# Kernel tuning notes

Hardware: AMD Instinct MI355X
Metric: run time of the kernel (lower is better)

The kernel has to match this reference:

```python
import jax, jax.numpy as jnp
import numpy as np

HIDDEN = 256
IN = 72  # 9*8
NUM_STEPS = 8


def setup_inputs() -> dict:
    key = jax.random.key(0)
    ks = jax.random.split(key, 12)
    s = 1.0 / np.sqrt(HIDDEN)
    B = 32768
    return {
        "z": jax.random.normal(ks[0], (1, B, HIDDEN), dtype=jnp.float32),
        # LSTM (torch layout): gates order i, f, g, o
        "W_ih": jax.random.uniform(ks[1], (4 * HIDDEN, IN), minval=-s, maxval=s),
        "W_hh": jax.random.uniform(ks[2], (4 * HIDDEN, HIDDEN), minval=-s, maxval=s),
        "b_ih": jax.random.uniform(ks[3], (4 * HIDDEN,), minval=-s, maxval=s),
        "b_hh": jax.random.uniform(ks[4], (4 * HIDDEN,), minval=-s, maxval=s),
        # Linear h: 256 -> 256
        "Wh": jax.random.uniform(ks[5], (HIDDEN, HIDDEN), minval=-s, maxval=s),
        "bh": jax.random.uniform(ks[6], (HIDDEN,), minval=-s, maxval=s),
        # Linear c: 256 -> 256
        "Wc": jax.random.uniform(ks[7], (HIDDEN, HIDDEN), minval=-s, maxval=s),
        "bc": jax.random.uniform(ks[8], (HIDDEN,), minval=-s, maxval=s),
        # Linear hout: 256 -> 72
        "Wo": jax.random.uniform(ks[9], (IN, HIDDEN), minval=-s, maxval=s),
        "bo": jax.random.uniform(ks[10], (IN,), minval=-s, maxval=s),
    }


def reference(z, W_ih, W_hh, b_ih, b_hh, Wh, bh, Wc, bc, Wo, bo):
    B = z.shape[1]
    z0 = z[0]                           # (B, 256)
    h = z0 @ Wh.T + bh                  # initial hidden state
    c = z0 @ Wc.T + bc                  # initial cell state
    x = jnp.zeros((B, IN), dtype=z.dtype)

    def step(carry, _):
        x, h, c = carry
        gates = x @ W_ih.T + b_ih + h @ W_hh.T + b_hh   # (B, 1024)
        i, f, g, o = jnp.split(gates, 4, axis=-1)
        i = jax.nn.sigmoid(i)
        f = jax.nn.sigmoid(f)
        g = jnp.tanh(g)
        o = jax.nn.sigmoid(o)
        c = f * c + i * g
        h = o * jnp.tanh(c)
        y = jax.nn.sigmoid(h @ Wo.T + bo)               # (B, 72), fed back as next input
        return (y, h, c), y

    _, ys = jax.lax.scan(step, (x, h, c), None, length=NUM_STEPS)  # (8, B, 72)
    return jnp.transpose(ys, (1, 0, 2))                             # (B, 8, 72)
```

## Files before the change

### kernel.cpp

```cpp
#include <hip/hip_runtime.h>
#include <hip/hip_bf16.h>

#define HID   256
#define NGATE 1024
#define INP   72
#define STEPS 8
#define TB    64
#define NTHR  1024
#define LDH   264
#define LDX   104

#define WSEQ2 32768
#define OFF_WHI 524288
#define OFF_WCI 589824
#define N_ALL   655360
#define OFF_BG_BYTES    1310720
#define OFF_STAGE_BYTES 1314816

typedef short  s8_t  __attribute__((ext_vector_type(8)));
typedef float  f4_t  __attribute__((ext_vector_type(4)));

static __device__ __forceinline__ unsigned short f2bf(float f) {
  unsigned int u = __float_as_uint(f);
  u = (u + 0x7FFFu + ((u >> 16) & 1u)) >> 16;
  return (unsigned short)u;
}
static __device__ __forceinline__ float fast_rcp(float x) {
#if __has_builtin(__builtin_amdgcn_rcpf)
  return __builtin_amdgcn_rcpf(x);
#else
  return 1.f / x;
#endif
}
static __device__ __forceinline__ float sigm(float x) {
  return fast_rcp(1.f + __expf(-x));
}
static __device__ __forceinline__ float tanh_(float x) {
  float t = fminf(-2.f * x, 88.f);
  float e = __expf(t);
  return (1.f - e) * fast_rcp(1.f + e);
}

__global__ void prep_kernel(const float* __restrict__ Wih, const float* __restrict__ Whh,
                            const float* __restrict__ bih, const float* __restrict__ bhh,
                            const float* __restrict__ Wh, const float* __restrict__ Wc,
                            const float* __restrict__ Wo,
                            unsigned short* __restrict__ wsh, float* __restrict__ bg) {
  int stride = gridDim.x * blockDim.x;
  for (int i = blockIdx.x * blockDim.x + threadIdx.x; i < N_ALL + NGATE; i += stride) {
    if (i < N_ALL) {
      float v = 0.f;
      if (i < OFF_WHI) {
        int w  = i >> 15;
        int r  = i & 32767;
        int f  = r >> 9;
        int e  = r & 511;
        int lane = e >> 3, j = e & 7;
        int lq = lane >> 4, ln = lane & 15;
        int kk = lq * 8 + j;
        if (f < 32) {
          int kc = f >> 2, q = f & 3;
          int g  = q * 256 + w * 16 + ln;
          int k  = kc * 32 + kk;
          v = Whh[g * HID + k];
        } else if (f < 44) {
          int t  = f - 32;
          int kc = t >> 2, q = t & 3;
          int g  = q * 256 + w * 16 + ln;
          int k  = kc * 32 + kk;
          v = (k < INP) ? Wih[g * INP + k] : 0.f;
        } else if (f < 52) {
          int kc = f - 44;
          int c  = w * 16 + ln;
          int k  = kc * 32 + kk;
          v = (w < 5 && c < INP) ? Wo[c * HID + k] : 0.f;
        }
      } else {
        int base = (i < OFF_WCI) ? OFF_WHI : OFF_WCI;
        const float* Wsrc = (i < OFF_WCI) ? Wh : Wc;
        int jj = i - base;
        int w  = jj >> 12;
        int r  = jj & 4095;
        int kc = r >> 9;
        int e  = r & 511;
        int lane = e >> 3, j = e & 7;
        int lq = lane >> 4, ln = lane & 15;
        int c  = w * 16 + ln;
        int k  = kc * 32 + lq * 8 + j;
        v = Wsrc[c * HID + k];
      }
      wsh[i] = f2bf(v);
    } else {
      int jb = i - N_ALL;
      bg[jb] = bih[jb] + bhh[jb];
    }
  }
}

template <int STAGED>
__global__ __launch_bounds__(NTHR, 4) void lstm_kernel(
    const float* __restrict__ z, const unsigned short* __restrict__ wsh,
    const float* __restrict__ bg, const float* __restrict__ bh,
    const float* __restrict__ bc, const float* __restrict__ bo,
    float* __restrict__ out, float* __restrict__ stage, int NB) {
  __shared__ unsigned short h_lds[TB * LDH];
  __shared__ unsigned short x_lds[TB * LDX];

  const int tid  = threadIdx.x;
  const int w    = tid >> 6;
  const int lane = tid & 63;
  const int lq   = lane >> 4;
  const int ln   = lane & 15;
  const int rb   = blockIdx.x * TB;
  const int colh0 = w * 16 + ln;

  const unsigned short* wst = wsh + w * WSEQ2 + lane * 8;
  const unsigned short* whi = wsh + OFF_WHI + w * 4096 + lane * 8;
  const unsigned short* wci = wsh + OFF_WCI + w * 4096 + lane * 8;
  const unsigned short* h_rd = &h_lds[ln * LDH + lq * 8];
  const unsigned short* x_rd = &x_lds[ln * LDX + lq * 8];
  unsigned short*       h_wr = &h_lds[(lq * 4) * LDH + colh0];

  for (int i = tid; i < TB * LDX; i += NTHR) x_lds[i] = 0;

  f4_t acc_h[4], acc_c[4];
  #pragma unroll
  for (int rt = 0; rt < 4; ++rt) {
    acc_h[rt] = {0.f, 0.f, 0.f, 0.f};
    acc_c[rt] = {0.f, 0.f, 0.f, 0.f};
  }

  const float* z_l = z + (size_t)(rb + ln) * HID + lq * 8;

  #pragma unroll 2
  for (int kc = 0; kc < 8; ++kc) {
    s8_t a[4];
    #pragma unroll
    for (int rt = 0; rt < 4; ++rt) {
      f4_t v0 = *reinterpret_cast<const f4_t*>(z_l + rt * 16 * HID + kc * 32);
      f4_t v1 = *reinterpret_cast<const f4_t*>(z_l + rt * 16 * HID + kc * 32 + 4);
      s8_t av;
      av[0] = (short)f2bf(v0[0]); av[1] = (short)f2bf(v0[1]);
      av[2] = (short)f2bf(v0[2]); av[3] = (short)f2bf(v0[3]);
      av[4] = (short)f2bf(v1[0]); av[5] = (short)f2bf(v1[1]);
      av[6] = (short)f2bf(v1[2]); av[7] = (short)f2bf(v1[3]);
      a[rt] = av;
    }
    s8_t bhf = *reinterpret_cast<const s8_t*>(whi + kc * 512);
    s8_t bcf = *reinterpret_cast<const s8_t*>(wci + kc * 512);
    #pragma unroll
    for (int rt = 0; rt < 4; ++rt) {
      acc_h[rt] = __builtin_amdgcn_mfma_f32_16x16x32_bf16(a[rt], bhf, acc_h[rt], 0, 0, 0);
      acc_c[rt] = __builtin_amdgcn_mfma_f32_16x16x32_bf16(a[rt], bcf, acc_c[rt], 0, 0, 0);
    }
  }

  float c_reg[4][4];
  {
    const float bhv = bh[colh0];
    const float bcv = bc[colh0];
    #pragma unroll
    for (int rt = 0; rt < 4; ++rt)
      #pragma unroll
      for (int r = 0; r < 4; ++r) {
        float hv = acc_h[rt][r] + bhv;
        c_reg[rt][r] = acc_c[rt][r] + bcv;
        h_wr[(rt * 16 + r) * LDH] = f2bf(hv);
      }
  }
  __syncthreads();

  float biasg[4];
  #pragma unroll
  for (int q = 0; q < 4; ++q)
    biasg[q] = bg[q * 256 + colh0];

  float bov = 0.f;
  if (w < 5 && colh0 < INP) bov = bo[colh0];

  for (int s = 0; s < STEPS; ++s) {
    f4_t acc[4][4];
    #pragma unroll
    for (int q = 0; q < 4; ++q)
      #pragma unroll
      for (int rt = 0; rt < 4; ++rt) {
        const float b = biasg[q];
        acc[q][rt] = {b, b, b, b};
      }

    #pragma unroll 2
    for (int kc = 0; kc < 8; ++kc) {
      s8_t a[4];
      #pragma unroll
      for (int rt = 0; rt < 4; ++rt)
        a[rt] = *reinterpret_cast<const s8_t*>(h_rd + rt * 16 * LDH + kc * 32);
      #pragma unroll
      for (int q = 0; q < 4; ++q) {
        s8_t bfr = *reinterpret_cast<const s8_t*>(wst + (kc * 4 + q) * 512);
        #pragma unroll
        for (int rt = 0; rt < 4; ++rt)
          acc[q][rt] = __builtin_amdgcn_mfma_f32_16x16x32_bf16(a[rt], bfr, acc[q][rt], 0, 0, 0);
      }
    }
    #pragma unroll
    for (int kc = 0; kc < 3; ++kc) {
      s8_t a[4];
      #pragma unroll
      for (int rt = 0; rt < 4; ++rt)
        a[rt] = *reinterpret_cast<const s8_t*>(x_rd + rt * 16 * LDX + kc * 32);
      #pragma unroll
      for (int q = 0; q < 4; ++q) {
        s8_t bfr = *reinterpret_cast<const s8_t*>(wst + (32 + kc * 4 + q) * 512);
        #pragma unroll
        for (int rt = 0; rt < 4; ++rt)
          acc[q][rt] = __builtin_amdgcn_mfma_f32_16x16x32_bf16(a[rt], bfr, acc[q][rt], 0, 0, 0);
      }
    }
    __syncthreads();

    #pragma unroll
    for (int rt = 0; rt < 4; ++rt)
      #pragma unroll
      for (int r = 0; r < 4; ++r) {
        float iv = sigm(acc[0][rt][r]);
        float fv = sigm(acc[1][rt][r]);
        float gv = tanh_(acc[2][rt][r]);
        float ov = sigm(acc[3][rt][r]);
        float cn = fv * c_reg[rt][r] + iv * gv;
        c_reg[rt][r] = cn;
        float hv = ov * tanh_(cn);
        h_wr[(rt * 16 + r) * LDH] = f2bf(hv);
      }
    __syncthreads();

    if (w < 5) {
      f4_t accy[4];
      #pragma unroll
      for (int rt = 0; rt < 4; ++rt) accy[rt] = {bov, bov, bov, bov};
      #pragma unroll 2
      for (int kc = 0; kc < 8; ++kc) {
        s8_t bfr = *reinterpret_cast<const s8_t*>(wst + (44 + kc) * 512);
        #pragma unroll
        for (int rt = 0; rt < 4; ++rt) {
          s8_t a = *reinterpret_cast<const s8_t*>(h_rd + rt * 16 * LDH + kc * 32);
          accy[rt] = __builtin_amdgcn_mfma_f32_16x16x32_bf16(a, bfr, accy[rt], 0, 0, 0);
        }
      }
      if (colh0 < INP) {
        float* st_base;
        if (STAGED) {
          st_base = stage + (((size_t)s * NB + blockIdx.x) * TB + lq * 4) * INP + colh0;
        } else {
          st_base = out + (size_t)(rb + lq * 4) * (STEPS * INP) + s * INP + colh0;
        }
        unsigned short* x_wr = &x_lds[(lq * 4) * LDX + colh0];
        #pragma unroll
        for (int rt = 0; rt < 4; ++rt)
          #pragma unroll
          for (int r = 0; r < 4; ++r) {
            float yv = sigm(accy[rt][r]);
            if (STAGED) {
              st_base[(size_t)(rt * 16 + r) * INP] = yv;
            } else {
              st_base[(size_t)(rt * 16 + r) * (STEPS * INP)] = yv;
            }
            x_wr[(rt * 16 + r) * LDX] = f2bf(yv);
          }
      }
    }
    __syncthreads();
  }
}

__global__ __launch_bounds__(512) void reorder_kernel(
    const float* __restrict__ stage, float* __restrict__ out, int NB) {
  const int lane = threadIdx.x & 63;
  const int row  = blockIdx.x * 8 + (threadIdx.x >> 6);
  const int b    = row >> 6;
  const int r    = row & 63;
  #pragma unroll
  for (int i = lane; i < STEPS * INP; i += 64) {
    int s = i / INP;
    int c = i - s * INP;
    out[(size_t)row * (STEPS * INP) + i] =
        stage[(((size_t)s * NB + b) * TB + r) * INP + c];
  }
}

extern "C" void kernel_launch(void* const* d_in, const int* in_sizes, int n_in,
                              void* d_out, int out_size, void* d_ws, size_t ws_size,
                              hipStream_t stream) {
  const float* z   = (const float*)d_in[0];
  const float* Wih = (const float*)d_in[1];
  const float* Whh = (const float*)d_in[2];
  const float* bih = (const float*)d_in[3];
  const float* bhh = (const float*)d_in[4];
  const float* Wh  = (const float*)d_in[5];
  const float* bh  = (const float*)d_in[6];
  const float* Wc  = (const float*)d_in[7];
  const float* bc  = (const float*)d_in[8];
  const float* Wo  = (const float*)d_in[9];
  const float* bo  = (const float*)d_in[10];
  float* out = (float*)d_out;

  unsigned short* wsh = (unsigned short*)d_ws;
  float* bg    = (float*)((char*)d_ws + OFF_BG_BYTES);
  float* stage = (float*)((char*)d_ws + OFF_STAGE_BYTES);

  const int B  = in_sizes[0] / HID;
  const int NB = B / TB;

  hipLaunchKernelGGL(prep_kernel, dim3(512), dim3(256), 0, stream,
                     Wih, Whh, bih, bhh, Wh, Wc, Wo, wsh, bg);

  const size_t stage_need = (size_t)OFF_STAGE_BYTES + (size_t)B * STEPS * INP * 4;
  if (ws_size >= stage_need) {
    hipLaunchKernelGGL((lstm_kernel<1>), dim3(NB), dim3(NTHR), 0, stream,
                       z, wsh, bg, bh, bc, bo, out, stage, NB);
    hipLaunchKernelGGL(reorder_kernel, dim3(B / 8), dim3(512), 0, stream,
                       stage, out, NB);
  } else {
    hipLaunchKernelGGL((lstm_kernel<0>), dim3(NB), dim3(NTHR), 0, stream,
                       z, wsh, bg, bh, bc, bo, out, stage, NB);
  }
}
```

Baseline: 557.0 us.

## Double-buffer LSTM hidden state in LDS to drop one barrier per step

Hidden state now ping-pongs between two LDS buffers, and the x buffer shares a unified LDS array with stride LDH. The h@W_hh product reads the current buffer and the new h is written to the other, so the barrier at the end of each step goes away and the x-part MFMAs now sit after the first barrier. The step loop is unrolled by two via a macro so buffer pointers are static. This raises LDS use (three 64x264 bf16 buffers), which could limit occupancy, and the synchronization correctness across steps is subtle.

```diff
diff --git a/kernel.cpp b/kernel.cpp
--- a/kernel.cpp
+++ b/kernel.cpp
@@ -8,7 +8,7 @@
 #define TB    64
 #define NTHR  1024
 #define LDH   264
-#define LDX   104
+#define ELEMS_BUF 16896
 
 #define WSEQ2 32768
 #define OFF_WHI 524288
@@ -97,14 +97,107 @@
   }
 }
 
+#define STEP(CUR_RD, NXT_RD, NXT_WR, SIDX)                                    \
+  {                                                                           \
+    f4_t acc[4][4];                                                           \
+    _Pragma("unroll")                                                         \
+    for (int q = 0; q < 4; ++q)                                               \
+      _Pragma("unroll")                                                       \
+      for (int rt = 0; rt < 4; ++rt) {                                        \
+        const float b = biasg[q];                                             \
+        acc[q][rt] = {b, b, b, b};                                            \
+      }                                                                       \
+     \
+    _Pragma("unroll 2")                                                       \
+    for (int kc = 0; kc < 8; ++kc) {                                          \
+      s8_t a[4];                                                              \
+      _Pragma("unroll")                                                       \
+      for (int rt = 0; rt < 4; ++rt)                                          \
+        a[rt] = *reinterpret_cast<const s8_t*>((CUR_RD) + rt * 16 * LDH + kc * 32); \
+      _Pragma("unroll")                                                       \
+      for (int q = 0; q < 4; ++q) {                                           \
+        s8_t bfr = *reinterpret_cast<const s8_t*>(wst + (kc * 4 + q) * 512);  \
+        _Pragma("unroll")                                                     \
+        for (int rt = 0; rt < 4; ++rt)                                        \
+          acc[q][rt] = __builtin_amdgcn_mfma_f32_16x16x32_bf16(a[rt], bfr, acc[q][rt], 0, 0, 0); \
+      }                                                                       \
+    }                                                                         \
+    __syncthreads();         \
+           \
+    _Pragma("unroll")                                                         \
+    for (int kc = 0; kc < 3; ++kc) {                                          \
+      s8_t a[4];                                                              \
+      _Pragma("unroll")                                                       \
+      for (int rt = 0; rt < 4; ++rt)                                          \
+        a[rt] = *reinterpret_cast<const s8_t*>(h_rdA + ELEMS_BUF + rt * 16 * LDH + kc * 32); \
+      _Pragma("unroll")                                                       \
+      for (int q = 0; q < 4; ++q) {                                           \
+        s8_t bfr = *reinterpret_cast<const s8_t*>(wst + (32 + kc * 4 + q) * 512); \
+        _Pragma("unroll")                                                     \
+        for (int rt = 0; rt < 4; ++rt)                                        \
+          acc[q][rt] = __builtin_amdgcn_mfma_f32_16x16x32_bf16(a[rt], bfr, acc[q][rt], 0, 0, 0); \
+      }                                                                       \
+    }                                                                         \
+       \
+    _Pragma("unroll")                                                         \
+    for (int rt = 0; rt < 4; ++rt)                                            \
+      _Pragma("unroll")                                                       \
+      for (int r = 0; r < 4; ++r) {                                           \
+        float iv = sigm(acc[0][rt][r]);                                       \
+        float fv = sigm(acc[1][rt][r]);                                       \
+        float gv = tanh_(acc[2][rt][r]);                                      \
+        float ov = sigm(acc[3][rt][r]);                                       \
+        float cn = fv * c_reg[rt][r] + iv * gv;                               \
+        c_reg[rt][r] = cn;                                                    \
+        float hv = ov * tanh_(cn);                                            \
+        (NXT_WR)[(rt * 16 + r) * LDH] = f2bf(hv);                             \
+      }                                                                       \
+    __syncthreads();                    \
+                       \
+    if (w < 5) {                                                              \
+      f4_t accy[4];                                                           \
+      _Pragma("unroll")                                                       \
+      for (int rt = 0; rt < 4; ++rt) accy[rt] = {bov, bov, bov, bov};         \
+      _Pragma("unroll 2")                                                     \
+      for (int kc = 0; kc < 8; ++kc) {                                        \
+        s8_t bfr = *reinterpret_cast<const s8_t*>(wst + (44 + kc) * 512);     \
+        _Pragma("unroll")                                                     \
+        for (int rt = 0; rt < 4; ++rt) {                                      \
+          s8_t a = *reinterpret_cast<const s8_t*>((NXT_RD) + rt * 16 * LDH + kc * 32); \
+          accy[rt] = __builtin_amdgcn_mfma_f32_16x16x32_bf16(a, bfr, accy[rt], 0, 0, 0); \
+        }                                                                     \
+      }                                                                       \
+      if (colh0 < INP) {                                                      \
+        float* st_base;                                                       \
+        if (STAGED) {                                                         \
+          st_base = stage + (((size_t)(SIDX) * NB + blockIdx.x) * TB + lq * 4) * INP + colh0; \
+        } else {                                                              \
+          st_base = out + (size_t)(rb + lq * 4) * (STEPS * INP) + (SIDX) * INP + colh0; \
+        }                                                                     \
+        unsigned short* x_wr = &lds[ELEMS_BUF + (lq * 4) * LDH + colh0];      \
+        _Pragma("unroll")                                                     \
+        for (int rt = 0; rt < 4; ++rt)                                        \
+          _Pragma("unroll")                                                   \
+          for (int r = 0; r < 4; ++r) {                                       \
+            float yv = sigm(accy[rt][r]);                                     \
+            if (STAGED) {                                                     \
+              st_base[(size_t)(rt * 16 + r) * INP] = yv;                      \
+            } else {                                                          \
+              st_base[(size_t)(rt * 16 + r) * (STEPS * INP)] = yv;            \
+            }                                                                 \
+            x_wr[(rt * 16 + r) * LDH] = f2bf(yv);                             \
+          }                                                                   \
+      }                                                                       \
+    }                                                                         \
+  }
+
 template <int STAGED>
 __global__ __launch_bounds__(NTHR, 4) void lstm_kernel(
     const float* __restrict__ z, const unsigned short* __restrict__ wsh,
     const float* __restrict__ bg, const float* __restrict__ bh,
     const float* __restrict__ bc, const float* __restrict__ bo,
     float* __restrict__ out, float* __restrict__ stage, int NB) {
-  __shared__ unsigned short h_lds[TB * LDH];
-  __shared__ unsigned short x_lds[TB * LDX];
+  __shared__ unsigned short lds[3 * ELEMS_BUF];
 
   const int tid  = threadIdx.x;
   const int w    = tid >> 6;
@@ -117,11 +210,13 @@
   const unsigned short* wst = wsh + w * WSEQ2 + lane * 8;
   const unsigned short* whi = wsh + OFF_WHI + w * 4096 + lane * 8;
   const unsigned short* wci = wsh + OFF_WCI + w * 4096 + lane * 8;
-  const unsigned short* h_rd = &h_lds[ln * LDH + lq * 8];
-  const unsigned short* x_rd = &x_lds[ln * LDX + lq * 8];
-  unsigned short*       h_wr = &h_lds[(lq * 4) * LDH + colh0];
-
-  for (int i = tid; i < TB * LDX; i += NTHR) x_lds[i] = 0;
+
+  const unsigned short* h_rdA = &lds[ln * LDH + lq * 8];
+  const unsigned short* h_rdB = h_rdA + 2 * ELEMS_BUF;
+  unsigned short*       h_wrA = &lds[(lq * 4) * LDH + colh0];
+  unsigned short*       h_wrB = h_wrA + 2 * ELEMS_BUF;
+
+  for (int i = tid; i < ELEMS_BUF; i += NTHR) lds[ELEMS_BUF + i] = 0;
 
   f4_t acc_h[4], acc_c[4];
   #pragma unroll
@@ -165,10 +260,9 @@
       for (int r = 0; r < 4; ++r) {
         float hv = acc_h[rt][r] + bhv;
         c_reg[rt][r] = acc_c[rt][r] + bcv;
-        h_wr[(rt * 16 + r) * LDH] = f2bf(hv);
+        h_wrA[(rt * 16 + r) * LDH] = f2bf(hv);
       }
   }
-  __syncthreads();
 
   float biasg[4];
   #pragma unroll
@@ -178,97 +272,12 @@
   float bov = 0.f;
   if (w < 5 && colh0 < INP) bov = bo[colh0];
 
-  for (int s = 0; s < STEPS; ++s) {
-    f4_t acc[4][4];
-    #pragma unroll
-    for (int q = 0; q < 4; ++q)
-      #pragma unroll
-      for (int rt = 0; rt < 4; ++rt) {
-        const float b = biasg[q];
-        acc[q][rt] = {b, b, b, b};
-      }
-
-    #pragma unroll 2
-    for (int kc = 0; kc < 8; ++kc) {
-      s8_t a[4];
-      #pragma unroll
-      for (int rt = 0; rt < 4; ++rt)
-        a[rt] = *reinterpret_cast<const s8_t*>(h_rd + rt * 16 * LDH + kc * 32);
-      #pragma unroll
-      for (int q = 0; q < 4; ++q) {
-        s8_t bfr = *reinterpret_cast<const s8_t*>(wst + (kc * 4 + q) * 512);
-        #pragma unroll
-        for (int rt = 0; rt < 4; ++rt)
-          acc[q][rt] = __builtin_amdgcn_mfma_f32_16x16x32_bf16(a[rt], bfr, acc[q][rt], 0, 0, 0);
-      }
-    }
-    #pragma unroll
-    for (int kc = 0; kc < 3; ++kc) {
-      s8_t a[4];
-      #pragma unroll
-      for (int rt = 0; rt < 4; ++rt)
-        a[rt] = *reinterpret_cast<const s8_t*>(x_rd + rt * 16 * LDX + kc * 32);
-      #pragma unroll
-      for (int q = 0; q < 4; ++q) {
-        s8_t bfr = *reinterpret_cast<const s8_t*>(wst + (32 + kc * 4 + q) * 512);
-        #pragma unroll
-        for (int rt = 0; rt < 4; ++rt)
-          acc[q][rt] = __builtin_amdgcn_mfma_f32_16x16x32_bf16(a[rt], bfr, acc[q][rt], 0, 0, 0);
-      }
-    }
-    __syncthreads();
-
-    #pragma unroll
-    for (int rt = 0; rt < 4; ++rt)
-      #pragma unroll
-      for (int r = 0; r < 4; ++r) {
-        float iv = sigm(acc[0][rt][r]);
-        float fv = sigm(acc[1][rt][r]);
-        float gv = tanh_(acc[2][rt][r]);
-        float ov = sigm(acc[3][rt][r]);
-        float cn = fv * c_reg[rt][r] + iv * gv;
-        c_reg[rt][r] = cn;
-        float hv = ov * tanh_(cn);
-        h_wr[(rt * 16 + r) * LDH] = f2bf(hv);
-      }
-    __syncthreads();
-
-    if (w < 5) {
-      f4_t accy[4];
-      #pragma unroll
-      for (int rt = 0; rt < 4; ++rt) accy[rt] = {bov, bov, bov, bov};
-      #pragma unroll 2
-      for (int kc = 0; kc < 8; ++kc) {
-        s8_t bfr = *reinterpret_cast<const s8_t*>(wst + (44 + kc) * 512);
-        #pragma unroll
-        for (int rt = 0; rt < 4; ++rt) {
-          s8_t a = *reinterpret_cast<const s8_t*>(h_rd + rt * 16 * LDH + kc * 32);
-          accy[rt] = __builtin_amdgcn_mfma_f32_16x16x32_bf16(a, bfr, accy[rt], 0, 0, 0);
-        }
-      }
-      if (colh0 < INP) {
-        float* st_base;
-        if (STAGED) {
-          st_base = stage + (((size_t)s * NB + blockIdx.x) * TB + lq * 4) * INP + colh0;
-        } else {
-          st_base = out + (size_t)(rb + lq * 4) * (STEPS * INP) + s * INP + colh0;
-        }
-        unsigned short* x_wr = &x_lds[(lq * 4) * LDX + colh0];
-        #pragma unroll
-        for (int rt = 0; rt < 4; ++rt)
-          #pragma unroll
-          for (int r = 0; r < 4; ++r) {
-            float yv = sigm(accy[rt][r]);
-            if (STAGED) {
-              st_base[(size_t)(rt * 16 + r) * INP] = yv;
-            } else {
-              st_base[(size_t)(rt * 16 + r) * (STEPS * INP)] = yv;
-            }
-            x_wr[(rt * 16 + r) * LDX] = f2bf(yv);
-          }
-      }
-    }
-    __syncthreads();
+  __syncthreads();
+
+  #pragma unroll 1
+  for (int s2 = 0; s2 < STEPS; s2 += 2) {
+    STEP(h_rdA, h_rdB, h_wrB, s2);
+    STEP(h_rdB, h_rdA, h_wrA, s2 + 1);
   }
 }
 
```

Result: slower. 591.8 us (+6.3%).
